# Performance work log

Measured on AMD Instinct MI355X. Metric: run time of the kernel, lower is better.

The kernel has to match this reference:

```python
import jax, jax.numpy as jnp
import numpy as np

N = 50000          # nodes
E = 1_600_000      # edges
H = 64             # agg_hidden (heads=1, concat)
IN = 7             # in_channels
EDIM = 4           # edge_dim
G = 256            # num graphs in batch
FC = 128           # fc_hidden
NC = 2             # num_classes
SLOPE = 0.2        # GATv2 LeakyReLU negative slope


def setup_inputs() -> dict:
    key = jax.random.key(0)
    ks = jax.random.split(key, 24)
    s = 0.1
    d = {
        "x": jax.random.normal(ks[0], (N, IN), dtype=jnp.float32),
        "edge_index": jax.random.randint(ks[1], (2, E), 0, N, dtype=jnp.int32),
        "edge_attr": jax.random.normal(ks[2], (E, EDIM), dtype=jnp.float32),
        "batch": jnp.sort(jax.random.randint(ks[3], (N,), 0, G, dtype=jnp.int32)),
        # GATv2 layer 0 (in=7 -> 64)
        "Wl0": jax.random.normal(ks[4], (IN, H)) * s,
        "bl0": jnp.zeros((H,), jnp.float32),
        "Wr0": jax.random.normal(ks[5], (IN, H)) * s,
        "br0": jnp.zeros((H,), jnp.float32),
        "We0": jax.random.normal(ks[6], (EDIM, H)) * s,
        "att0": jax.random.normal(ks[7], (H,)) * s,
        "bias0": jnp.zeros((H,), jnp.float32),
        # GATv2 layer 1 (64 -> 64)
        "Wl1": jax.random.normal(ks[8], (H, H)) * s,
        "bl1": jnp.zeros((H,), jnp.float32),
        "Wr1": jax.random.normal(ks[9], (H, H)) * s,
        "br1": jnp.zeros((H,), jnp.float32),
        "We1": jax.random.normal(ks[10], (EDIM, H)) * s,
        "att1": jax.random.normal(ks[11], (H,)) * s,
        "bias1": jnp.zeros((H,), jnp.float32),
        # MLP head
        "fc1_w": jax.random.normal(ks[12], (H, FC)) * s,
        "fc1_b": jnp.zeros((FC,), jnp.float32),
        "fc2_w": jax.random.normal(ks[13], (FC, NC)) * s,
        "fc2_b": jnp.zeros((NC,), jnp.float32),
    }
    return d


def _gatv2(x, src, dst, edge_attr, Wl, bl, Wr, br, We, att, bias):
    # GATv2Conv (heads=1, concat=True, edge_dim=EDIM), eval mode (no dropout)
    xl = x @ Wl + bl                         # source-side projection [N,H]
    xr = x @ Wr + br                         # target-side projection [N,H]
    e = xl[src] + xr[dst] + edge_attr @ We   # per-edge pre-activation [E,H]
    score = jax.nn.leaky_relu(e, SLOPE) @ att  # [E]
    # segment softmax over destination nodes
    m = jax.ops.segment_max(score, dst, num_segments=N)
    ex = jnp.exp(score - m[dst])
    den = jax.ops.segment_sum(ex, dst, num_segments=N)
    alpha = ex / (den[dst] + 1e-16)
    out = jax.ops.segment_sum(xl[src] * alpha[:, None], dst, num_segments=N)
    return out + bias


def reference(x, edge_index, edge_attr, batch,
              Wl0, bl0, Wr0, br0, We0, att0, bias0,
              Wl1, bl1, Wr1, br1, We1, att1, bias1,
              fc1_w, fc1_b, fc2_w, fc2_b):
    src, dst = edge_index[0], edge_index[1]
    h = jax.nn.elu(_gatv2(x, src, dst, edge_attr, Wl0, bl0, Wr0, br0, We0, att0, bias0))
    h = jax.nn.elu(_gatv2(h, src, dst, edge_attr, Wl1, bl1, Wr1, br1, We1, att1, bias1))
    # global mean pool over graphs
    sums = jax.ops.segment_sum(h, batch, num_segments=G)
    cnt = jax.ops.segment_sum(jnp.ones((h.shape[0],), h.dtype), batch, num_segments=G)
    g = sums / jnp.maximum(cnt, 1.0)[:, None]      # [G,H]
    g = jax.nn.relu(g @ fc1_w + fc1_b)
    logits = g @ fc2_w + fc2_b
    return jax.nn.log_softmax(logits, axis=1)
```

## Files before the change

kernel.cpp:

```cpp
#include <hip/hip_runtime.h>
#include <hip/hip_fp16.h>

#define N_NODES 50000
#define N_EDGES 1600000
#define H 64
#define IN_CH 7
#define EDIM 4
#define G_GRAPHS 256
#define FC 128
#define NC 2
#define SLOPE 0.2f
#define NBUCK 196
#define EPB1 8192
#define NB1 ((N_EDGES + EPB1 - 1) / EPB1)
#define PAIR_BLOCKS ((N_NODES * 32 + 255) / 256)

typedef _Float16 h2v __attribute__((ext_vector_type(2)));

__device__ __forceinline__ float fdot2f(h2v a, h2v b, float c) {
#if defined(__has_builtin) && __has_builtin(__builtin_amdgcn_fdot2)
    return __builtin_amdgcn_fdot2(a, b, c, false);
#else
    return c + (float)a[0] * (float)b[0] + (float)a[1] * (float)b[1];
#endif
}

__device__ __forceinline__ float wave_sum_to63(float x) {
    x += __int_as_float(__builtin_amdgcn_update_dpp(0, __float_as_int(x), 0x111, 0xf, 0xf, true));
    x += __int_as_float(__builtin_amdgcn_update_dpp(0, __float_as_int(x), 0x112, 0xf, 0xf, true));
    x += __int_as_float(__builtin_amdgcn_update_dpp(0, __float_as_int(x), 0x114, 0xf, 0xf, true));
    x += __int_as_float(__builtin_amdgcn_update_dpp(0, __float_as_int(x), 0x118, 0xf, 0xf, true));
    x += __int_as_float(__builtin_amdgcn_update_dpp(0, __float_as_int(x), 0x142, 0xf, 0xf, true));
    x += __int_as_float(__builtin_amdgcn_update_dpp(0, __float_as_int(x), 0x143, 0xf, 0xf, true));
    return x;
}
__device__ __forceinline__ float lane63_bcast(float x) {
    return __int_as_float(__builtin_amdgcn_readlane(__float_as_int(x), 63));
}
__device__ __forceinline__ float readlane_f(float x, int i) {
    return __int_as_float(__builtin_amdgcn_readlane(__float_as_int(x), i));
}

__global__ __launch_bounds__(256) void front_kernel(
        const int* __restrict__ dst, int* __restrict__ rank1, int* __restrict__ bhist,
        const float* __restrict__ xin,
        const float* __restrict__ Wl0, const float* __restrict__ bl0,
        const float* __restrict__ Wr0, const float* __restrict__ br0,
        __half2* __restrict__ xlh, __half2* __restrict__ xrh,
        const float* __restrict__ We0, const float* __restrict__ We1,
        const float* __restrict__ Wl1, const float* __restrict__ bl1,
        const float* __restrict__ Wr1, const float* __restrict__ br1,
        __half2* __restrict__ weh0, __half2* __restrict__ weh1,
        __half2* __restrict__ wt, float* __restrict__ bb,
        const float* __restrict__ att0, const float* __restrict__ att1,
        __half2* __restrict__ atth0, __half2* __restrict__ atth1) {
    __shared__ int hist[NBUCK];
    int b = blockIdx.x;
    int t = threadIdx.x;
    if (b < NB1) {
        if (t < NBUCK) hist[t] = 0;
        __syncthreads();
#pragma unroll
        for (int i = 0; i < EPB1 / 256; ++i) {
            int e = b * EPB1 + i * 256 + t;
            if (e < N_EDGES) {
                int k = dst[e] >> 8;
                rank1[e] = atomicAdd(&hist[k], 1);
            }
        }
        __syncthreads();
        if (t < NBUCK) bhist[b * NBUCK + t] = hist[t];
    } else if (b < NB1 + PAIR_BLOCKS) {
        int idx = (b - NB1) * 256 + t;
        if (idx < N_NODES * 32) {
            int n = idx >> 5;
            int c = idx & 31;
            const float* xi = xin + n * IN_CH;
            float2 bl2 = ((const float2*)bl0)[c];
            float2 br2 = ((const float2*)br0)[c];
            float al0 = bl2.x, al1 = bl2.y, ar0 = br2.x, ar1 = br2.y;
#pragma unroll
            for (int k = 0; k < IN_CH; ++k) {
                float xv = xi[k];
                float2 wl2 = ((const float2*)(Wl0 + k * H))[c];
                float2 wr2 = ((const float2*)(Wr0 + k * H))[c];
                al0 += xv * wl2.x; al1 += xv * wl2.y;
                ar0 += xv * wr2.x; ar1 += xv * wr2.y;
            }
            xlh[idx] = __floats2half2_rn(al0, al1);
            xrh[idx] = __floats2half2_rn(ar0, ar1);
        }
    } else {
        if (t < 32) {
            for (int k = 0; k < 4; ++k)
                weh0[t * 4 + k] = __floats2half2_rn(We0[k * H + 2 * t], We0[k * H + 2 * t + 1]);
        } else if (t < 64) {
            int c = t - 32;
            for (int k = 0; k < 4; ++k)
                weh1[c * 4 + k] = __floats2half2_rn(We1[k * H + 2 * c], We1[k * H + 2 * c + 1]);
        }
        if (t < 128) {
            const float* W = (t < 64) ? Wl1 : Wr1;
            int c = t & 63;
            for (int kk = 0; kk < 32; ++kk)
                wt[t * 32 + kk] = __floats2half2_rn(W[(2 * kk) * H + c], W[(2 * kk + 1) * H + c]);
            bb[t] = (t < 64) ? bl1[c] : br1[c];
        } else if (t < 160) {
            int c = t - 128;
            atth0[c] = __floats2half2_rn(att0[2 * c], att0[2 * c + 1]);
            atth1[c] = __floats2half2_rn(att1[2 * c], att1[2 * c + 1]);
        }
    }
}

__global__ __launch_bounds__(256) void bucket_scan_kernel(
        const int* __restrict__ bhist, int* __restrict__ bases, int* __restrict__ cb_start) {
    __shared__ int lds[256];
    int t = threadIdx.x;
    int run = 0;
    if (t < NBUCK) {
        for (int b = 0; b < NB1; ++b) {
            bases[b * NBUCK + t] = run;
            run += bhist[b * NBUCK + t];
        }
    }
    lds[t] = (t < NBUCK) ? run : 0;
    __syncthreads();
    for (int off = 1; off < 256; off <<= 1) {
        int x = (t >= off) ? lds[t - off] : 0;
        __syncthreads();
        lds[t] += x;
        __syncthreads();
    }
    if (t < NBUCK) cb_start[t] = lds[t] - run;
    if (t == NBUCK - 1) cb_start[NBUCK] = lds[t];
}

__global__ void coarse_scatter_kernel(const int* __restrict__ src, const int* __restrict__ dst,
                                      const int* __restrict__ rank1, const int* __restrict__ bases,
                                      const int* __restrict__ cb_start,
                                      const float* __restrict__ edge_attr,
                                      int4* __restrict__ tmp) {
    int e = blockIdx.x * blockDim.x + threadIdx.x;
    if (e >= N_EDGES) return;
    int d = dst[e];
    int k = d >> 8;
    int b = e / EPB1;
    int slot = cb_start[k] + bases[b * NBUCK + k] + rank1[e];
    float4 ea = ((const float4*)edge_attr)[e];
    __half2 h01 = __floats2half2_rn(ea.x, ea.y);
    __half2 h23 = __floats2half2_rn(ea.z, ea.w);
    int4 ent;
    ent.x = src[e];
    ent.y = *reinterpret_cast<int*>(&h01);
    ent.z = *reinterpret_cast<int*>(&h23);
    ent.w = d;
    tmp[slot] = ent;
}

__global__ __launch_bounds__(256) void fine_sort_kernel(
        const int* __restrict__ cb_start, const int4* __restrict__ tmp,
        int4* __restrict__ csr, int* __restrict__ srcs,
        int* __restrict__ row_start) {
    __shared__ int hist2[256];
    __shared__ int cursor[256];
    __shared__ int lds[256];
    int k = blockIdx.x;
    int t = threadIdx.x;
    int beg = cb_start[k], end = cb_start[k + 1];
    hist2[t] = 0;
    __syncthreads();
    for (int i = beg + t; i < end; i += 256)
        atomicAdd(&hist2[tmp[i].w & 255], 1);
    __syncthreads();
    int v = hist2[t];
    lds[t] = v;
    __syncthreads();
    for (int off = 1; off < 256; off <<= 1) {
        int x = (t >= off) ? lds[t - off] : 0;
        __syncthreads();
        lds[t] += x;
        __syncthreads();
    }
    int pre = lds[t] - v;
    cursor[t] = pre;
    int node = k * 256 + t;
    if (node <= N_NODES) row_start[node] = beg + pre;
    __syncthreads();
    for (int i = beg + t; i < end; i += 256) {
        int4 ent = tmp[i];
        int slot = beg + atomicAdd(&cursor[ent.w & 255], 1);
        csr[slot] = ent;
        srcs[slot] = ent.x;
    }
}

__global__ __launch_bounds__(256) void proj1_kernel(
        const float* __restrict__ xin,
        const __half2* __restrict__ wt,
        const float* __restrict__ bb,
        __half2* __restrict__ xlh, __half2* __restrict__ xrh) {
    int g = __builtin_amdgcn_readfirstlane((int)(threadIdx.x >> 6));
    int lane = threadIdx.x & 63;
    int node = blockIdx.x * 64 + lane;
    if (node >= N_NODES) return;

    h2v xrow[32];
    const float4* xp = (const float4*)(xin + node * 64);
#pragma unroll
    for (int q = 0; q < 16; ++q) {
        float4 v = xp[q];
        __half2 a = __floats2half2_rn(v.x, v.y);
        __half2 b = __floats2half2_rn(v.z, v.w);
        xrow[2 * q]     = *reinterpret_cast<h2v*>(&a);
        xrow[2 * q + 1] = *reinterpret_cast<h2v*>(&b);
    }

    __half2* outp = (g < 2) ? xlh : xrh;
    int chbase = g * 32;
    int localbase = (g & 1) * 16;

#pragma unroll
    for (int cp = 0; cp < 16; ++cp) {
        int ch0 = chbase + 2 * cp;
        const h2v* w0 = (const h2v*)(wt + ch0 * 32);
        const h2v* w1 = (const h2v*)(wt + (ch0 + 1) * 32);
        float a0 = bb[ch0], a1 = bb[ch0 + 1];
#pragma unroll
        for (int kk = 0; kk < 32; ++kk) {
            a0 = fdot2f(xrow[kk], w0[kk], a0);
            a1 = fdot2f(xrow[kk], w1[kk], a1);
        }
        outp[node * 32 + localbase + cp] = __floats2half2_rn(a0, a1);
    }
}

__global__ __launch_bounds__(256) void score_kernel(
        const int4* __restrict__ csr,
        const __half2* __restrict__ xlh, const __half2* __restrict__ xrh,
        const __half2* __restrict__ weh, const __half2* __restrict__ atth,
        float* __restrict__ score) {
    int t = threadIdx.x;
    int e = blockIdx.x * 256 + t;
    int4 ent = csr[e];
    __half2 ea01 = *reinterpret_cast<__half2*>(&ent.y);
    __half2 ea23 = *reinterpret_cast<__half2*>(&ent.z);
    __half2 e0 = __half2half2(__low2half(ea01));
    __half2 e1 = __half2half2(__high2half(ea01));
    __half2 e2 = __half2half2(__low2half(ea23));
    __half2 e3 = __half2half2(__high2half(ea23));
    const h2v sl = { (_Float16)SLOPE, (_Float16)SLOPE };
    const int4* xa = (const int4*)(xlh + ent.x * 32);
    const int4* xb = (const int4*)(xrh + ent.w * 32);
    float acc0 = 0.f, acc1 = 0.f;
#pragma unroll
    for (int k = 0; k < 8; ++k) {
        int4 va = xa[k];
        int4 vb = xb[k];
        const __half2* ha = reinterpret_cast<const __half2*>(&va);
        const __half2* hc = reinterpret_cast<const __half2*>(&vb);
#pragma unroll
        for (int j = 0; j < 4; ++j) {
            int c = k * 4 + j;
            __half2 v2 = __hadd2(ha[j], hc[j]);
            v2 = __hfma2(e0, weh[c * 4 + 0], v2);
            v2 = __hfma2(e1, weh[c * 4 + 1], v2);
            v2 = __hfma2(e2, weh[c * 4 + 2], v2);
            v2 = __hfma2(e3, weh[c * 4 + 3], v2);
            h2v vv = *reinterpret_cast<h2v*>(&v2);
            h2v Lv = __builtin_elementwise_max(vv, sl * vv);
            __half2 av = atth[c];
            if (j & 1)
                acc1 = fdot2f(Lv, *reinterpret_cast<h2v*>(&av), acc1);
            else
                acc0 = fdot2f(Lv, *reinterpret_cast<h2v*>(&av), acc0);
        }
    }
    score[e] = acc0 + acc1;
}

__global__ __launch_bounds__(256) void agg_kernel(
        const int* __restrict__ row_start,
        const int* __restrict__ srcs,
        const float* __restrict__ score,
        const __half2* __restrict__ xlh,
        const float* __restrict__ bias,
        float* __restrict__ out) {
    int wave = (blockIdx.x * blockDim.x + threadIdx.x) >> 6;
    if (wave >= N_NODES) return;
    int lane = threadIdx.x & 63;
    int c = lane & 31;
    int hb = lane >> 5;
    int d = wave;
    int beg = __builtin_amdgcn_readfirstlane(row_start[d]);
    int end = __builtin_amdgcn_readfirstlane(row_start[d + 1]);

    float l_lane = 0.f;
    float ax0 = 0.f, ay0 = 0.f, ax1 = 0.f, ay1 = 0.f;

    for (int cbeg = beg; cbeg < end; cbeg += 64) {
        int n = end - cbeg;
        float sc = score[cbeg + lane];
        float p = __expf(sc);
        p = (lane < n) ? p : 0.f;
        l_lane += p;

        int nn = min(n, 64);
        int j = 0;
        for (; j + 4 <= nn; j += 4) {
            int sA0 = __builtin_amdgcn_readfirstlane(srcs[cbeg + j + 0]);
            int sB0 = __builtin_amdgcn_readfirstlane(srcs[cbeg + j + 1]);
            int sA1 = __builtin_amdgcn_readfirstlane(srcs[cbeg + j + 2]);
            int sB1 = __builtin_amdgcn_readfirstlane(srcs[cbeg + j + 3]);
            float pA0 = readlane_f(p, j + 0), pB0 = readlane_f(p, j + 1);
            float pA1 = readlane_f(p, j + 2), pB1 = readlane_f(p, j + 3);
            int s0 = hb ? sB0 : sA0;
            int s1 = hb ? sB1 : sA1;
            float pv0 = hb ? pB0 : pA0;
            float pv1 = hb ? pB1 : pA1;
            float2 x0 = __half22float2(xlh[s0 * 32 + c]);
            float2 x1 = __half22float2(xlh[s1 * 32 + c]);
            ax0 += pv0 * x0.x; ay0 += pv0 * x0.y;
            ax1 += pv1 * x1.x; ay1 += pv1 * x1.y;
        }
        for (; j + 2 <= nn; j += 2) {
            int sA = __builtin_amdgcn_readfirstlane(srcs[cbeg + j + 0]);
            int sB = __builtin_amdgcn_readfirstlane(srcs[cbeg + j + 1]);
            float pA = readlane_f(p, j + 0), pB = readlane_f(p, j + 1);
            int s = hb ? sB : sA;
            float pv = hb ? pB : pA;
            float2 xf = __half22float2(xlh[s * 32 + c]);
            ax0 += pv * xf.x; ay0 += pv * xf.y;
        }
        if (j < nn) {
            int sA = __builtin_amdgcn_readfirstlane(srcs[cbeg + j]);
            float pA = readlane_f(p, j);
            float pv = hb ? 0.f : pA;
            float2 xf = __half22float2(xlh[sA * 32 + c]);
            ax0 += pv * xf.x; ay0 += pv * xf.y;
        }
    }

    float l = lane63_bcast(wave_sum_to63(l_lane));
    float accx = ax0 + ax1, accy = ay0 + ay1;
    accx += __shfl_xor(accx, 32, 64);
    accy += __shfl_xor(accy, 32, 64);
    if (hb == 0) {
        float inv = 1.f / (l + 1e-16f);
        float2 b2 = ((const float2*)bias)[c];
        float o0 = accx * inv + b2.x;
        float o1 = accy * inv + b2.y;
        o0 = o0 > 0.f ? o0 : expm1f(o0);
        o1 = o1 > 0.f ? o1 : expm1f(o1);
        ((float2*)out)[d * 32 + c] = float2{o0, o1};
    }
}

__global__ __launch_bounds__(256) void pool_head_kernel(
        const float* __restrict__ h, const int* __restrict__ batch,
        const float* __restrict__ fc1w, const float* __restrict__ fc1b,
        const float* __restrict__ fc2w, const float* __restrict__ fc2b,
        float* __restrict__ out) {
    int g = blockIdx.x;
    int lo = 0, hi = N_NODES;
    while (lo < hi) { int mid = (lo + hi) >> 1; if (batch[mid] < g) lo = mid + 1; else hi = mid; }
    int start = lo;
    hi = N_NODES;
    while (lo < hi) { int mid = (lo + hi) >> 1; if (batch[mid] < g + 1) lo = mid + 1; else hi = mid; }
    int end = lo;

    int lane = threadIdx.x & 63;
    int w = threadIdx.x >> 6;
    float s = 0.f;
    for (int n = start + w; n < end; n += 4) s += h[n * H + lane];
    __shared__ float red[4][H];
    __shared__ float gv[H];
    __shared__ float f[FC];
    __shared__ float lg[NC];
    red[w][lane] = s;
    __syncthreads();
    if (w == 0) {
        float tot = red[0][lane] + red[1][lane] + red[2][lane] + red[3][lane];
        gv[lane] = tot / fmaxf((float)(end - start), 1.f);
    }
    __syncthreads();
    int t = threadIdx.x;
    if (t < FC) {
        float acc = fc1b[t];
#pragma unroll 16
        for (int k = 0; k < H; ++k) acc += gv[k] * fc1w[k * FC + t];
        f[t] = fmaxf(acc, 0.f);
    }
    __syncthreads();
    if (t < NC) {
        float a = fc2b[t];
        for (int k = 0; k < FC; ++k) a += f[k] * fc2w[k * NC + t];
        lg[t] = a;
    }
    __syncthreads();
    if (t < NC) {
        float mx = fmaxf(lg[0], lg[1]);
        float lse = mx + logf(expf(lg[0] - mx) + expf(lg[1] - mx));
        out[g * NC + t] = lg[t] - lse;
    }
}

extern "C" void kernel_launch(void* const* d_in, const int* in_sizes, int n_in,
                              void* d_out, int out_size, void* d_ws, size_t ws_size,
                              hipStream_t stream) {
    const float* x         = (const float*)d_in[0];
    const int*   edge_idx  = (const int*)d_in[1];
    const float* edge_attr = (const float*)d_in[2];
    const int*   batch     = (const int*)d_in[3];
    const float* Wl0  = (const float*)d_in[4];
    const float* bl0  = (const float*)d_in[5];
    const float* Wr0  = (const float*)d_in[6];
    const float* br0  = (const float*)d_in[7];
    const float* We0  = (const float*)d_in[8];
    const float* att0 = (const float*)d_in[9];
    const float* bias0= (const float*)d_in[10];
    const float* Wl1  = (const float*)d_in[11];
    const float* bl1  = (const float*)d_in[12];
    const float* Wr1  = (const float*)d_in[13];
    const float* br1  = (const float*)d_in[14];
    const float* We1  = (const float*)d_in[15];
    const float* att1 = (const float*)d_in[16];
    const float* bias1= (const float*)d_in[17];
    const float* fc1w = (const float*)d_in[18];
    const float* fc1b = (const float*)d_in[19];
    const float* fc2w = (const float*)d_in[20];
    const float* fc2b = (const float*)d_in[21];

    const int NH = N_NODES * H;
    __half2* xlh    = (__half2*)d_ws;
    __half2* xrh    = xlh + N_NODES * 32;
    float* C        = (float*)(xrh + N_NODES * 32);
    float* escore   = C + NH;
    float* pad      = escore + N_EDGES;
    int4*  tmp      = (int4*)C;
    int4*  csr      = (int4*)(pad + N_EDGES);
    int*   srcs     = (int*)(csr + N_EDGES);
    int*   row_start= srcs + N_EDGES;
    unsigned* m_enc = (unsigned*)(row_start + N_NODES + 1);
    int*   rank1    = (int*)(m_enc + N_NODES);
    int*   bhist    = rank1 + N_EDGES;
    int*   bases    = bhist + NB1 * NBUCK;
    int*   cb_start = bases + NB1 * NBUCK;
    __half2* weh0   = (__half2*)(cb_start + NBUCK + 1);
    __half2* weh1   = weh0 + 128;
    __half2* wt1    = weh1 + 128;
    float* bb1      = (float*)(wt1 + 128 * 32);
    __half2* atth0  = (__half2*)(bb1 + 128);
    __half2* atth1  = atth0 + 32;

    const int* src = edge_idx;
    const int* dst = edge_idx + N_EDGES;

    const int edgeBlocks = (N_EDGES + 255) / 256;
    const int waveBlocks = (N_NODES * 64 + 255) / 256;
    const int p1Blocks   = (N_NODES + 63) / 64;
    const int frontBlocks = NB1 + PAIR_BLOCKS + 1;

    front_kernel<<<frontBlocks, 256, 0, stream>>>(dst, rank1, bhist,
                                                  x, Wl0, bl0, Wr0, br0, xlh, xrh,
                                                  We0, We1, Wl1, bl1, Wr1, br1,
                                                  weh0, weh1, wt1, bb1,
                                                  att0, att1, atth0, atth1);
    bucket_scan_kernel<<<1, 256, 0, stream>>>(bhist, bases, cb_start);
    coarse_scatter_kernel<<<edgeBlocks, 256, 0, stream>>>(src, dst, rank1, bases, cb_start,
                                                          edge_attr, tmp);
    fine_sort_kernel<<<NBUCK, 256, 0, stream>>>(cb_start, tmp, csr, srcs, row_start);

    score_kernel<<<edgeBlocks, 256, 0, stream>>>(csr, xlh, xrh, weh0, atth0, escore);
    agg_kernel<<<waveBlocks, 256, 0, stream>>>(row_start, srcs, escore, xlh, bias0, C);

    proj1_kernel<<<p1Blocks, 256, 0, stream>>>(C, wt1, bb1, xlh, xrh);
    score_kernel<<<edgeBlocks, 256, 0, stream>>>(csr, xlh, xrh, weh1, atth1, escore);
    agg_kernel<<<waveBlocks, 256, 0, stream>>>(row_start, srcs, escore, xlh, bias1, C);

    pool_head_kernel<<<G_GRAPHS, 256, 0, stream>>>(C, batch, fc1w, fc1b, fc2w, fc2b, (float*)d_out);
}
```

Baseline: 411.8 us.

## Fuse edge score computation into per-node aggregation and drop srcs array

Edge attention scores are now computed inside the per-destination wave aggregation kernel instead of a separate per-edge score kernel. This drops the score buffer's write and read and the separate srcs array. Source indices come from the loaded CSR entries via readlane. The destination's xr row is loaded once per wave rather than once per edge. The trade-off is idle or redundant lanes when a node has fewer than 64 edges, since out-of-range lanes repeat the last edge's work.

```diff
diff --git a/kernel.cpp b/kernel.cpp
--- a/kernel.cpp
+++ b/kernel.cpp
@@ -160,8 +160,7 @@
 
 __global__ __launch_bounds__(256) void fine_sort_kernel(
         const int* __restrict__ cb_start, const int4* __restrict__ tmp,
-        int4* __restrict__ csr, int* __restrict__ srcs,
-        int* __restrict__ row_start) {
+        int4* __restrict__ csr, int* __restrict__ row_start) {
     __shared__ int hist2[256];
     __shared__ int cursor[256];
     __shared__ int lds[256];
@@ -191,7 +190,6 @@
         int4 ent = tmp[i];
         int slot = beg + atomicAdd(&cursor[ent.w & 255], 1);
         csr[slot] = ent;
-        srcs[slot] = ent.x;
     }
 }
 
@@ -235,55 +233,11 @@
     }
 }
 
-__global__ __launch_bounds__(256) void score_kernel(
+__global__ __launch_bounds__(256) void fused_agg_kernel(
+        const int* __restrict__ row_start,
         const int4* __restrict__ csr,
         const __half2* __restrict__ xlh, const __half2* __restrict__ xrh,
         const __half2* __restrict__ weh, const __half2* __restrict__ atth,
-        float* __restrict__ score) {
-    int t = threadIdx.x;
-    int e = blockIdx.x * 256 + t;
-    int4 ent = csr[e];
-    __half2 ea01 = *reinterpret_cast<__half2*>(&ent.y);
-    __half2 ea23 = *reinterpret_cast<__half2*>(&ent.z);
-    __half2 e0 = __half2half2(__low2half(ea01));
-    __half2 e1 = __half2half2(__high2half(ea01));
-    __half2 e2 = __half2half2(__low2half(ea23));
-    __half2 e3 = __half2half2(__high2half(ea23));
-    const h2v sl = { (_Float16)SLOPE, (_Float16)SLOPE };
-    const int4* xa = (const int4*)(xlh + ent.x * 32);
-    const int4* xb = (const int4*)(xrh + ent.w * 32);
-    float acc0 = 0.f, acc1 = 0.f;
-#pragma unroll
-    for (int k = 0; k < 8; ++k) {
-        int4 va = xa[k];
-        int4 vb = xb[k];
-        const __half2* ha = reinterpret_cast<const __half2*>(&va);
-        const __half2* hc = reinterpret_cast<const __half2*>(&vb);
-#pragma unroll
-        for (int j = 0; j < 4; ++j) {
-            int c = k * 4 + j;
-            __half2 v2 = __hadd2(ha[j], hc[j]);
-            v2 = __hfma2(e0, weh[c * 4 + 0], v2);
-            v2 = __hfma2(e1, weh[c * 4 + 1], v2);
-            v2 = __hfma2(e2, weh[c * 4 + 2], v2);
-            v2 = __hfma2(e3, weh[c * 4 + 3], v2);
-            h2v vv = *reinterpret_cast<h2v*>(&v2);
-            h2v Lv = __builtin_elementwise_max(vv, sl * vv);
-            __half2 av = atth[c];
-            if (j & 1)
-                acc1 = fdot2f(Lv, *reinterpret_cast<h2v*>(&av), acc1);
-            else
-                acc0 = fdot2f(Lv, *reinterpret_cast<h2v*>(&av), acc0);
-        }
-    }
-    score[e] = acc0 + acc1;
-}
-
-__global__ __launch_bounds__(256) void agg_kernel(
-        const int* __restrict__ row_start,
-        const int* __restrict__ srcs,
-        const float* __restrict__ score,
-        const __half2* __restrict__ xlh,
         const float* __restrict__ bias,
         float* __restrict__ out) {
     int wave = (blockIdx.x * blockDim.x + threadIdx.x) >> 6;
@@ -295,23 +249,61 @@
     int beg = __builtin_amdgcn_readfirstlane(row_start[d]);
     int end = __builtin_amdgcn_readfirstlane(row_start[d + 1]);
 
+    const h2v sl = { (_Float16)SLOPE, (_Float16)SLOPE };
+    const int4* xb = (const int4*)(xrh + (size_t)d * 32);
+
     float l_lane = 0.f;
     float ax0 = 0.f, ay0 = 0.f, ax1 = 0.f, ay1 = 0.f;
 
     for (int cbeg = beg; cbeg < end; cbeg += 64) {
         int n = end - cbeg;
-        float sc = score[cbeg + lane];
-        float p = __expf(sc);
+        int nn = min(n, 64);
+
+        int idx = cbeg + lane;
+        idx = idx < end ? idx : end - 1;
+        int4 ent = csr[idx];
+        __half2 ea01 = *reinterpret_cast<__half2*>(&ent.y);
+        __half2 ea23 = *reinterpret_cast<__half2*>(&ent.z);
+        __half2 e0 = __half2half2(__low2half(ea01));
+        __half2 e1 = __half2half2(__high2half(ea01));
+        __half2 e2 = __half2half2(__low2half(ea23));
+        __half2 e3 = __half2half2(__high2half(ea23));
+        const int4* xa = (const int4*)(xlh + (size_t)ent.x * 32);
+        float acc0 = 0.f, acc1 = 0.f;
+#pragma unroll
+        for (int k = 0; k < 8; ++k) {
+            int4 va = xa[k];
+            int4 vb = xb[k];
+            const __half2* ha = reinterpret_cast<const __half2*>(&va);
+            const __half2* hc = reinterpret_cast<const __half2*>(&vb);
+#pragma unroll
+            for (int j = 0; j < 4; ++j) {
+                int cc = k * 4 + j;
+                __half2 v2 = __hadd2(ha[j], hc[j]);
+                v2 = __hfma2(e0, weh[cc * 4 + 0], v2);
+                v2 = __hfma2(e1, weh[cc * 4 + 1], v2);
+                v2 = __hfma2(e2, weh[cc * 4 + 2], v2);
+                v2 = __hfma2(e3, weh[cc * 4 + 3], v2);
+                h2v vv = *reinterpret_cast<h2v*>(&v2);
+                h2v Lv = __builtin_elementwise_max(vv, sl * vv);
+                __half2 av = atth[cc];
+                if (j & 1)
+                    acc1 = fdot2f(Lv, *reinterpret_cast<h2v*>(&av), acc1);
+                else
+                    acc0 = fdot2f(Lv, *reinterpret_cast<h2v*>(&av), acc0);
+            }
+        }
+        float p = __expf(acc0 + acc1);
         p = (lane < n) ? p : 0.f;
         l_lane += p;
-
-        int nn = min(n, 64);
+        int esrc = ent.x;
+
         int j = 0;
         for (; j + 4 <= nn; j += 4) {
-            int sA0 = __builtin_amdgcn_readfirstlane(srcs[cbeg + j + 0]);
-            int sB0 = __builtin_amdgcn_readfirstlane(srcs[cbeg + j + 1]);
-            int sA1 = __builtin_amdgcn_readfirstlane(srcs[cbeg + j + 2]);
-            int sB1 = __builtin_amdgcn_readfirstlane(srcs[cbeg + j + 3]);
+            int sA0 = __builtin_amdgcn_readlane(esrc, j + 0);
+            int sB0 = __builtin_amdgcn_readlane(esrc, j + 1);
+            int sA1 = __builtin_amdgcn_readlane(esrc, j + 2);
+            int sB1 = __builtin_amdgcn_readlane(esrc, j + 3);
             float pA0 = readlane_f(p, j + 0), pB0 = readlane_f(p, j + 1);
             float pA1 = readlane_f(p, j + 2), pB1 = readlane_f(p, j + 3);
             int s0 = hb ? sB0 : sA0;
@@ -324,8 +316,8 @@
             ax1 += pv1 * x1.x; ay1 += pv1 * x1.y;
         }
         for (; j + 2 <= nn; j += 2) {
-            int sA = __builtin_amdgcn_readfirstlane(srcs[cbeg + j + 0]);
-            int sB = __builtin_amdgcn_readfirstlane(srcs[cbeg + j + 1]);
+            int sA = __builtin_amdgcn_readlane(esrc, j + 0);
+            int sB = __builtin_amdgcn_readlane(esrc, j + 1);
             float pA = readlane_f(p, j + 0), pB = readlane_f(p, j + 1);
             int s = hb ? sB : sA;
             float pv = hb ? pB : pA;
@@ -333,7 +325,7 @@
             ax0 += pv * xf.x; ay0 += pv * xf.y;
         }
         if (j < nn) {
-            int sA = __builtin_amdgcn_readfirstlane(srcs[cbeg + j]);
+            int sA = __builtin_amdgcn_readlane(esrc, j);
             float pA = readlane_f(p, j);
             float pv = hb ? 0.f : pA;
             float2 xf = __half22float2(xlh[sA * 32 + c]);
@@ -469,14 +461,14 @@
     bucket_scan_kernel<<<1, 256, 0, stream>>>(bhist, bases, cb_start);
     coarse_scatter_kernel<<<edgeBlocks, 256, 0, stream>>>(src, dst, rank1, bases, cb_start,
                                                           edge_attr, tmp);
-    fine_sort_kernel<<<NBUCK, 256, 0, stream>>>(cb_start, tmp, csr, srcs, row_start);
-
-    score_kernel<<<edgeBlocks, 256, 0, stream>>>(csr, xlh, xrh, weh0, atth0, escore);
-    agg_kernel<<<waveBlocks, 256, 0, stream>>>(row_start, srcs, escore, xlh, bias0, C);
+    fine_sort_kernel<<<NBUCK, 256, 0, stream>>>(cb_start, tmp, csr, row_start);
+
+    fused_agg_kernel<<<waveBlocks, 256, 0, stream>>>(row_start, csr, xlh, xrh,
+                                                     weh0, atth0, bias0, C);
 
     proj1_kernel<<<p1Blocks, 256, 0, stream>>>(C, wt1, bb1, xlh, xrh);
-    score_kernel<<<edgeBlocks, 256, 0, stream>>>(csr, xlh, xrh, weh1, atth1, escore);
-    agg_kernel<<<waveBlocks, 256, 0, stream>>>(row_start, srcs, escore, xlh, bias1, C);
+    fused_agg_kernel<<<waveBlocks, 256, 0, stream>>>(row_start, csr, xlh, xrh,
+                                                     weh1, atth1, bias1, C);
 
     pool_head_kernel<<<G_GRAPHS, 256, 0, stream>>>(C, batch, fc1w, fc1b, fc2w, fc2b, (float*)d_out);
 }
```

Measured after the change: 450.3 us. 9.4% more time.

## Fuse layer-0 edge scoring into fine sort and widen sort blocks to 1024

Applied to the files above, without the earlier changes.

Layer-0 attention scores are now computed inside the fine-sort kernel as each edge is placed, which removes a separate score kernel launch and its re-read of the CSR array. The fine-sort blocks grow from 256 to 1024 threads so that 196 blocks carry more parallelism for the heavier per-edge work. The workspace is reorganised so escore aliases the rank1 buffer, which is dead by then. The trade-off is that the fused kernel runs on only 196 blocks with scattered gathers, so it may get less memory-level parallelism than the standalone edge-parallel score kernel had.

```diff
diff --git a/kernel.cpp b/kernel.cpp
--- a/kernel.cpp
+++ b/kernel.cpp
@@ -39,6 +39,45 @@
 }
 __device__ __forceinline__ float readlane_f(float x, int i) {
     return __int_as_float(__builtin_amdgcn_readlane(__float_as_int(x), i));
+}
+
+__device__ __forceinline__ float gat_score(int4 ent,
+        const __half2* __restrict__ xlh, const __half2* __restrict__ xrh,
+        const __half2* __restrict__ weh, const __half2* __restrict__ atth) {
+    __half2 ea01 = *reinterpret_cast<__half2*>(&ent.y);
+    __half2 ea23 = *reinterpret_cast<__half2*>(&ent.z);
+    __half2 e0 = __half2half2(__low2half(ea01));
+    __half2 e1 = __half2half2(__high2half(ea01));
+    __half2 e2 = __half2half2(__low2half(ea23));
+    __half2 e3 = __half2half2(__high2half(ea23));
+    const h2v sl = { (_Float16)SLOPE, (_Float16)SLOPE };
+    const int4* xa = (const int4*)(xlh + (size_t)ent.x * 32);
+    const int4* xb = (const int4*)(xrh + (size_t)ent.w * 32);
+    float acc0 = 0.f, acc1 = 0.f;
+#pragma unroll
+    for (int k = 0; k < 8; ++k) {
+        int4 va = xa[k];
+        int4 vb = xb[k];
+        const __half2* ha = reinterpret_cast<const __half2*>(&va);
+        const __half2* hc = reinterpret_cast<const __half2*>(&vb);
+#pragma unroll
+        for (int j = 0; j < 4; ++j) {
+            int c = k * 4 + j;
+            __half2 v2 = __hadd2(ha[j], hc[j]);
+            v2 = __hfma2(e0, weh[c * 4 + 0], v2);
+            v2 = __hfma2(e1, weh[c * 4 + 1], v2);
+            v2 = __hfma2(e2, weh[c * 4 + 2], v2);
+            v2 = __hfma2(e3, weh[c * 4 + 3], v2);
+            h2v vv = *reinterpret_cast<h2v*>(&v2);
+            h2v Lv = __builtin_elementwise_max(vv, sl * vv);
+            __half2 av = atth[c];
+            if (j & 1)
+                acc1 = fdot2f(Lv, *reinterpret_cast<h2v*>(&av), acc1);
+            else
+                acc0 = fdot2f(Lv, *reinterpret_cast<h2v*>(&av), acc0);
+        }
+    }
+    return acc0 + acc1;
 }
 
 __global__ __launch_bounds__(256) void front_kernel(
@@ -158,40 +197,46 @@
     tmp[slot] = ent;
 }
 
-__global__ __launch_bounds__(256) void fine_sort_kernel(
+__global__ __launch_bounds__(1024) void fine_sort_kernel(
         const int* __restrict__ cb_start, const int4* __restrict__ tmp,
+        const __half2* __restrict__ xlh, const __half2* __restrict__ xrh,
+        const __half2* __restrict__ weh, const __half2* __restrict__ atth,
         int4* __restrict__ csr, int* __restrict__ srcs,
-        int* __restrict__ row_start) {
+        int* __restrict__ row_start, float* __restrict__ escore) {
     __shared__ int hist2[256];
     __shared__ int cursor[256];
     __shared__ int lds[256];
     int k = blockIdx.x;
     int t = threadIdx.x;
     int beg = cb_start[k], end = cb_start[k + 1];
-    hist2[t] = 0;
-    __syncthreads();
-    for (int i = beg + t; i < end; i += 256)
+    if (t < 256) hist2[t] = 0;
+    __syncthreads();
+    for (int i = beg + t; i < end; i += 1024)
         atomicAdd(&hist2[tmp[i].w & 255], 1);
     __syncthreads();
-    int v = hist2[t];
-    lds[t] = v;
+    int v = (t < 256) ? hist2[t] : 0;
+    if (t < 256) lds[t] = v;
     __syncthreads();
     for (int off = 1; off < 256; off <<= 1) {
-        int x = (t >= off) ? lds[t - off] : 0;
-        __syncthreads();
-        lds[t] += x;
-        __syncthreads();
-    }
-    int pre = lds[t] - v;
-    cursor[t] = pre;
-    int node = k * 256 + t;
-    if (node <= N_NODES) row_start[node] = beg + pre;
-    __syncthreads();
-    for (int i = beg + t; i < end; i += 256) {
+        int x = 0;
+        if (t < 256 && t >= off) x = lds[t - off];
+        __syncthreads();
+        if (t < 256) lds[t] += x;
+        __syncthreads();
+    }
+    if (t < 256) {
+        int pre = lds[t] - v;
+        cursor[t] = pre;
+        int node = k * 256 + t;
+        if (node <= N_NODES) row_start[node] = beg + pre;
+    }
+    __syncthreads();
+    for (int i = beg + t; i < end; i += 1024) {
         int4 ent = tmp[i];
         int slot = beg + atomicAdd(&cursor[ent.w & 255], 1);
         csr[slot] = ent;
         srcs[slot] = ent.x;
+        escore[slot] = gat_score(ent, xlh, xrh, weh, atth);
     }
 }
 
@@ -240,43 +285,8 @@
         const __half2* __restrict__ xlh, const __half2* __restrict__ xrh,
         const __half2* __restrict__ weh, const __half2* __restrict__ atth,
         float* __restrict__ score) {
-    int t = threadIdx.x;
-    int e = blockIdx.x * 256 + t;
-    int4 ent = csr[e];
-    __half2 ea01 = *reinterpret_cast<__half2*>(&ent.y);
-    __half2 ea23 = *reinterpret_cast<__half2*>(&ent.z);
-    __half2 e0 = __half2half2(__low2half(ea01));
-    __half2 e1 = __half2half2(__high2half(ea01));
-    __half2 e2 = __half2half2(__low2half(ea23));
-    __half2 e3 = __half2half2(__high2half(ea23));
-    const h2v sl = { (_Float16)SLOPE, (_Float16)SLOPE };
-    const int4* xa = (const int4*)(xlh + ent.x * 32);
-    const int4* xb = (const int4*)(xrh + ent.w * 32);
-    float acc0 = 0.f, acc1 = 0.f;
-#pragma unroll
-    for (int k = 0; k < 8; ++k) {
-        int4 va = xa[k];
-        int4 vb = xb[k];
-        const __half2* ha = reinterpret_cast<const __half2*>(&va);
-        const __half2* hc = reinterpret_cast<const __half2*>(&vb);
-#pragma unroll
-        for (int j = 0; j < 4; ++j) {
-            int c = k * 4 + j;
-            __half2 v2 = __hadd2(ha[j], hc[j]);
-            v2 = __hfma2(e0, weh[c * 4 + 0], v2);
-            v2 = __hfma2(e1, weh[c * 4 + 1], v2);
-            v2 = __hfma2(e2, weh[c * 4 + 2], v2);
-            v2 = __hfma2(e3, weh[c * 4 + 3], v2);
-            h2v vv = *reinterpret_cast<h2v*>(&v2);
-            h2v Lv = __builtin_elementwise_max(vv, sl * vv);
-            __half2 av = atth[c];
-            if (j & 1)
-                acc1 = fdot2f(Lv, *reinterpret_cast<h2v*>(&av), acc1);
-            else
-                acc0 = fdot2f(Lv, *reinterpret_cast<h2v*>(&av), acc0);
-        }
-    }
-    score[e] = acc0 + acc1;
+    int e = blockIdx.x * 256 + threadIdx.x;
+    score[e] = gat_score(csr[e], xlh, xrh, weh, atth);
 }
 
 __global__ __launch_bounds__(256) void agg_kernel(
@@ -431,18 +441,15 @@
     const float* fc2w = (const float*)d_in[20];
     const float* fc2b = (const float*)d_in[21];
 
-    const int NH = N_NODES * H;
     __half2* xlh    = (__half2*)d_ws;
     __half2* xrh    = xlh + N_NODES * 32;
     float* C        = (float*)(xrh + N_NODES * 32);
-    float* escore   = C + NH;
-    float* pad      = escore + N_EDGES;
     int4*  tmp      = (int4*)C;
-    int4*  csr      = (int4*)(pad + N_EDGES);
+    int4*  csr      = (int4*)(tmp + N_EDGES);
     int*   srcs     = (int*)(csr + N_EDGES);
     int*   row_start= srcs + N_EDGES;
-    unsigned* m_enc = (unsigned*)(row_start + N_NODES + 1);
-    int*   rank1    = (int*)(m_enc + N_NODES);
+    int*   rank1    = row_start + N_NODES + 1;
+    float* escore   = (float*)rank1;
     int*   bhist    = rank1 + N_EDGES;
     int*   bases    = bhist + NB1 * NBUCK;
     int*   cb_start = bases + NB1 * NBUCK;
@@ -469,9 +476,9 @@
     bucket_scan_kernel<<<1, 256, 0, stream>>>(bhist, bases, cb_start);
     coarse_scatter_kernel<<<edgeBlocks, 256, 0, stream>>>(src, dst, rank1, bases, cb_start,
                                                           edge_attr, tmp);
-    fine_sort_kernel<<<NBUCK, 256, 0, stream>>>(cb_start, tmp, csr, srcs, row_start);
-
-    score_kernel<<<edgeBlocks, 256, 0, stream>>>(csr, xlh, xrh, weh0, atth0, escore);
+    fine_sort_kernel<<<NBUCK, 1024, 0, stream>>>(cb_start, tmp, xlh, xrh, weh0, atth0,
+                                                 csr, srcs, row_start, escore);
+
     agg_kernel<<<waveBlocks, 256, 0, stream>>>(row_start, srcs, escore, xlh, bias0, C);
 
     proj1_kernel<<<p1Blocks, 256, 0, stream>>>(C, wt1, bb1, xlh, xrh);
```

Measured after the change: 444.6 us. +8.0%, slower.

## Use 64-node buckets and parallel two-stage scan for edge counting sort

Applied to the files above, without the earlier changes.

Bucket width for the two-pass counting sort by destination drops from 256 nodes to 64, which gives 782 buckets. The single-block serial bucket scan is replaced by a per-bucket parallel scan across edge blocks plus a second 1024-thread scan over bucket totals. Smaller buckets give the fine sort more blocks and shorter scans. The cost is larger shared-memory histograms in the front kernel, more global bhist/bases traffic and an extra launch. The score computation is moved into a helper function with no change in behaviour.

```diff
diff --git a/kernel.cpp b/kernel.cpp
--- a/kernel.cpp
+++ b/kernel.cpp
@@ -10,7 +10,9 @@
 #define FC 128
 #define NC 2
 #define SLOPE 0.2f
-#define NBUCK 196
+#define BSH 6
+#define BNODES 64
+#define NBUCK ((N_NODES + BNODES - 1) / BNODES)
 #define EPB1 8192
 #define NB1 ((N_EDGES + EPB1 - 1) / EPB1)
 #define PAIR_BLOCKS ((N_NODES * 32 + 255) / 256)
@@ -39,6 +41,45 @@
 }
 __device__ __forceinline__ float readlane_f(float x, int i) {
     return __int_as_float(__builtin_amdgcn_readlane(__float_as_int(x), i));
+}
+
+__device__ __forceinline__ float gat_score(int4 ent,
+        const __half2* __restrict__ xlh, const __half2* __restrict__ xrh,
+        const __half2* __restrict__ weh, const __half2* __restrict__ atth) {
+    __half2 ea01 = *reinterpret_cast<__half2*>(&ent.y);
+    __half2 ea23 = *reinterpret_cast<__half2*>(&ent.z);
+    __half2 e0 = __half2half2(__low2half(ea01));
+    __half2 e1 = __half2half2(__high2half(ea01));
+    __half2 e2 = __half2half2(__low2half(ea23));
+    __half2 e3 = __half2half2(__high2half(ea23));
+    const h2v sl = { (_Float16)SLOPE, (_Float16)SLOPE };
+    const int4* xa = (const int4*)(xlh + (size_t)ent.x * 32);
+    const int4* xb = (const int4*)(xrh + (size_t)ent.w * 32);
+    float acc0 = 0.f, acc1 = 0.f;
+#pragma unroll
+    for (int k = 0; k < 8; ++k) {
+        int4 va = xa[k];
+        int4 vb = xb[k];
+        const __half2* ha = reinterpret_cast<const __half2*>(&va);
+        const __half2* hc = reinterpret_cast<const __half2*>(&vb);
+#pragma unroll
+        for (int j = 0; j < 4; ++j) {
+            int c = k * 4 + j;
+            __half2 v2 = __hadd2(ha[j], hc[j]);
+            v2 = __hfma2(e0, weh[c * 4 + 0], v2);
+            v2 = __hfma2(e1, weh[c * 4 + 1], v2);
+            v2 = __hfma2(e2, weh[c * 4 + 2], v2);
+            v2 = __hfma2(e3, weh[c * 4 + 3], v2);
+            h2v vv = *reinterpret_cast<h2v*>(&v2);
+            h2v Lv = __builtin_elementwise_max(vv, sl * vv);
+            __half2 av = atth[c];
+            if (j & 1)
+                acc1 = fdot2f(Lv, *reinterpret_cast<h2v*>(&av), acc1);
+            else
+                acc0 = fdot2f(Lv, *reinterpret_cast<h2v*>(&av), acc0);
+        }
+    }
+    return acc0 + acc1;
 }
 
 __global__ __launch_bounds__(256) void front_kernel(
@@ -58,18 +99,18 @@
     int b = blockIdx.x;
     int t = threadIdx.x;
     if (b < NB1) {
-        if (t < NBUCK) hist[t] = 0;
+        for (int i = t; i < NBUCK; i += 256) hist[i] = 0;
         __syncthreads();
 #pragma unroll
         for (int i = 0; i < EPB1 / 256; ++i) {
             int e = b * EPB1 + i * 256 + t;
             if (e < N_EDGES) {
-                int k = dst[e] >> 8;
+                int k = dst[e] >> BSH;
                 rank1[e] = atomicAdd(&hist[k], 1);
             }
         }
         __syncthreads();
-        if (t < NBUCK) bhist[b * NBUCK + t] = hist[t];
+        for (int i = t; i < NBUCK; i += 256) bhist[b * NBUCK + i] = hist[i];
     } else if (b < NB1 + PAIR_BLOCKS) {
         int idx = (b - NB1) * 256 + t;
         if (idx < N_NODES * 32) {
@@ -113,18 +154,13 @@
     }
 }
 
-__global__ __launch_bounds__(256) void bucket_scan_kernel(
-        const int* __restrict__ bhist, int* __restrict__ bases, int* __restrict__ cb_start) {
+__global__ __launch_bounds__(256) void scan_a_kernel(
+        const int* __restrict__ bhist, int* __restrict__ bases, int* __restrict__ btot) {
     __shared__ int lds[256];
+    int k = blockIdx.x;
     int t = threadIdx.x;
-    int run = 0;
-    if (t < NBUCK) {
-        for (int b = 0; b < NB1; ++b) {
-            bases[b * NBUCK + t] = run;
-            run += bhist[b * NBUCK + t];
-        }
-    }
-    lds[t] = (t < NBUCK) ? run : 0;
+    int v = (t < NB1) ? bhist[t * NBUCK + k] : 0;
+    lds[t] = v;
     __syncthreads();
     for (int off = 1; off < 256; off <<= 1) {
         int x = (t >= off) ? lds[t - off] : 0;
@@ -132,7 +168,24 @@
         lds[t] += x;
         __syncthreads();
     }
-    if (t < NBUCK) cb_start[t] = lds[t] - run;
+    if (t < NB1) bases[t * NBUCK + k] = lds[t] - v;
+    if (t == NB1 - 1) btot[k] = lds[t];
+}
+
+__global__ __launch_bounds__(1024) void scan_b_kernel(
+        const int* __restrict__ btot, int* __restrict__ cb_start) {
+    __shared__ int lds[1024];
+    int t = threadIdx.x;
+    int v = (t < NBUCK) ? btot[t] : 0;
+    lds[t] = v;
+    __syncthreads();
+    for (int off = 1; off < 1024; off <<= 1) {
+        int x = (t >= off) ? lds[t - off] : 0;
+        __syncthreads();
+        lds[t] += x;
+        __syncthreads();
+    }
+    if (t < NBUCK) cb_start[t] = lds[t] - v;
     if (t == NBUCK - 1) cb_start[NBUCK] = lds[t];
 }
 
@@ -144,7 +197,7 @@
     int e = blockIdx.x * blockDim.x + threadIdx.x;
     if (e >= N_EDGES) return;
     int d = dst[e];
-    int k = d >> 8;
+    int k = d >> BSH;
     int b = e / EPB1;
     int slot = cb_start[k] + bases[b * NBUCK + k] + rank1[e];
     float4 ea = ((const float4*)edge_attr)[e];
@@ -162,34 +215,36 @@
         const int* __restrict__ cb_start, const int4* __restrict__ tmp,
         int4* __restrict__ csr, int* __restrict__ srcs,
         int* __restrict__ row_start) {
-    __shared__ int hist2[256];
-    __shared__ int cursor[256];
-    __shared__ int lds[256];
+    __shared__ int hist2[BNODES];
+    __shared__ int cursor[BNODES];
+    __shared__ int lds[BNODES];
     int k = blockIdx.x;
     int t = threadIdx.x;
     int beg = cb_start[k], end = cb_start[k + 1];
-    hist2[t] = 0;
+    if (t < BNODES) hist2[t] = 0;
     __syncthreads();
     for (int i = beg + t; i < end; i += 256)
-        atomicAdd(&hist2[tmp[i].w & 255], 1);
-    __syncthreads();
-    int v = hist2[t];
-    lds[t] = v;
-    __syncthreads();
-    for (int off = 1; off < 256; off <<= 1) {
-        int x = (t >= off) ? lds[t - off] : 0;
-        __syncthreads();
-        lds[t] += x;
-        __syncthreads();
-    }
-    int pre = lds[t] - v;
-    cursor[t] = pre;
-    int node = k * 256 + t;
-    if (node <= N_NODES) row_start[node] = beg + pre;
+        atomicAdd(&hist2[tmp[i].w & (BNODES - 1)], 1);
+    __syncthreads();
+    int v = 0;
+    if (t < BNODES) { v = hist2[t]; lds[t] = v; }
+    __syncthreads();
+    for (int off = 1; off < BNODES; off <<= 1) {
+        int x = (t < BNODES && t >= off) ? lds[t - off] : 0;
+        __syncthreads();
+        if (t < BNODES) lds[t] += x;
+        __syncthreads();
+    }
+    if (t < BNODES) {
+        int pre = lds[t] - v;
+        cursor[t] = pre;
+        int node = (k << BSH) + t;
+        if (node <= N_NODES) row_start[node] = beg + pre;
+    }
     __syncthreads();
     for (int i = beg + t; i < end; i += 256) {
         int4 ent = tmp[i];
-        int slot = beg + atomicAdd(&cursor[ent.w & 255], 1);
+        int slot = beg + atomicAdd(&cursor[ent.w & (BNODES - 1)], 1);
         csr[slot] = ent;
         srcs[slot] = ent.x;
     }
@@ -240,43 +295,8 @@
         const __half2* __restrict__ xlh, const __half2* __restrict__ xrh,
         const __half2* __restrict__ weh, const __half2* __restrict__ atth,
         float* __restrict__ score) {
-    int t = threadIdx.x;
-    int e = blockIdx.x * 256 + t;
-    int4 ent = csr[e];
-    __half2 ea01 = *reinterpret_cast<__half2*>(&ent.y);
-    __half2 ea23 = *reinterpret_cast<__half2*>(&ent.z);
-    __half2 e0 = __half2half2(__low2half(ea01));
-    __half2 e1 = __half2half2(__high2half(ea01));
-    __half2 e2 = __half2half2(__low2half(ea23));
-    __half2 e3 = __half2half2(__high2half(ea23));
-    const h2v sl = { (_Float16)SLOPE, (_Float16)SLOPE };
-    const int4* xa = (const int4*)(xlh + ent.x * 32);
-    const int4* xb = (const int4*)(xrh + ent.w * 32);
-    float acc0 = 0.f, acc1 = 0.f;
-#pragma unroll
-    for (int k = 0; k < 8; ++k) {
-        int4 va = xa[k];
-        int4 vb = xb[k];
-        const __half2* ha = reinterpret_cast<const __half2*>(&va);
-        const __half2* hc = reinterpret_cast<const __half2*>(&vb);
-#pragma unroll
-        for (int j = 0; j < 4; ++j) {
-            int c = k * 4 + j;
-            __half2 v2 = __hadd2(ha[j], hc[j]);
-            v2 = __hfma2(e0, weh[c * 4 + 0], v2);
-            v2 = __hfma2(e1, weh[c * 4 + 1], v2);
-            v2 = __hfma2(e2, weh[c * 4 + 2], v2);
-            v2 = __hfma2(e3, weh[c * 4 + 3], v2);
-            h2v vv = *reinterpret_cast<h2v*>(&v2);
-            h2v Lv = __builtin_elementwise_max(vv, sl * vv);
-            __half2 av = atth[c];
-            if (j & 1)
-                acc1 = fdot2f(Lv, *reinterpret_cast<h2v*>(&av), acc1);
-            else
-                acc0 = fdot2f(Lv, *reinterpret_cast<h2v*>(&av), acc0);
-        }
-    }
-    score[e] = acc0 + acc1;
+    int e = blockIdx.x * 256 + threadIdx.x;
+    score[e] = gat_score(csr[e], xlh, xrh, weh, atth);
 }
 
 __global__ __launch_bounds__(256) void agg_kernel(
@@ -431,21 +451,20 @@
     const float* fc2w = (const float*)d_in[20];
     const float* fc2b = (const float*)d_in[21];
 
-    const int NH = N_NODES * H;
     __half2* xlh    = (__half2*)d_ws;
     __half2* xrh    = xlh + N_NODES * 32;
     float* C        = (float*)(xrh + N_NODES * 32);
-    float* escore   = C + NH;
+    float* escore   = C + N_NODES * 64;
     float* pad      = escore + N_EDGES;
     int4*  tmp      = (int4*)C;
     int4*  csr      = (int4*)(pad + N_EDGES);
     int*   srcs     = (int*)(csr + N_EDGES);
     int*   row_start= srcs + N_EDGES;
-    unsigned* m_enc = (unsigned*)(row_start + N_NODES + 1);
-    int*   rank1    = (int*)(m_enc + N_NODES);
+    int*   rank1    = row_start + N_NODES + 1;
     int*   bhist    = rank1 + N_EDGES;
     int*   bases    = bhist + NB1 * NBUCK;
-    int*   cb_start = bases + NB1 * NBUCK;
+    int*   btot     = bases + NB1 * NBUCK;
+    int*   cb_start = btot + NBUCK;
     __half2* weh0   = (__half2*)(cb_start + NBUCK + 1);
     __half2* weh1   = weh0 + 128;
     __half2* wt1    = weh1 + 128;
@@ -466,7 +485,8 @@
                                                   We0, We1, Wl1, bl1, Wr1, br1,
                                                   weh0, weh1, wt1, bb1,
                                                   att0, att1, atth0, atth1);
-    bucket_scan_kernel<<<1, 256, 0, stream>>>(bhist, bases, cb_start);
+    scan_a_kernel<<<NBUCK, 256, 0, stream>>>(bhist, bases, btot);
+    scan_b_kernel<<<1, 1024, 0, stream>>>(btot, cb_start);
     coarse_scatter_kernel<<<edgeBlocks, 256, 0, stream>>>(src, dst, rank1, bases, cb_start,
                                                           edge_attr, tmp);
     fine_sort_kernel<<<NBUCK, 256, 0, stream>>>(cb_start, tmp, csr, srcs, row_start);
```

New measurement: 397.7 us. 3.4% less time.
